# Kernel optimization log

Measured on AMD Instinct MI355X. Metric: run time of the kernel, lower is better.

## Reference

```python
import jax, jax.numpy as jnp
import numpy as np

N_E = 16384
SPLIT = (512, 512)
BETA = 0.25
K = 10
B = 4096


def _l2n(x):
    # F.normalize(p=2, dim=-1)
    return x * jax.lax.rsqrt(jnp.sum(x * x, axis=-1, keepdims=True) + 1e-12)


def _dist(x, y):
    return (jnp.sum(x * x, axis=1, keepdims=True)
            + jnp.sum(y * y, axis=1)
            - 2.0 * jnp.einsum('bd,nd->bn', x, y))


def _usage(idx):
    counts = jnp.zeros((N_E,), jnp.float32).at[idx.reshape(-1)].add(1.0)
    return jnp.sum(counts > 0).astype(jnp.float32) / N_E


def _soft_topk(d, emb):
    # smallest-K distances -> softmax(-values) weighted codebook mix
    neg_vals, idx = jax.lax.top_k(-d, K)            # [B, K]
    w = jax.nn.softmax(neg_vals, axis=1)            # softmax(-values)
    z_q = jnp.einsum('bk,bkd->bd', w, emb[idx])     # gather + weighted sum
    return z_q, idx


def _losses(z_q, z):
    vq = jnp.mean((z_q - jax.lax.stop_gradient(z)) ** 2)
    commit = BETA * jnp.mean((jax.lax.stop_gradient(z_q) - z) ** 2)
    return vq, commit


def setup_inputs() -> dict:
    key = jax.random.key(0)
    ks = jax.random.split(key, 5)
    u = 1.0 / N_E
    return {
        'z': jax.random.normal(ks[0], (B, sum(SPLIT)), jnp.float32),
        'w_text': jax.random.uniform(ks[1], (N_E, SPLIT[0]), jnp.float32, -u, u),
        'w_graph': jax.random.uniform(ks[2], (N_E, SPLIT[1]), jnp.float32, -u, u),
        'w_shared_text': jax.random.uniform(ks[3], (N_E, SPLIT[0]), jnp.float32, -u, u),
        'w_shared_graph': jax.random.uniform(ks[4], (N_E, SPLIT[1]), jnp.float32, -u, u),
    }


def reference(z, w_text, w_graph, w_shared_text, w_shared_graph):
    z_text, z_graph = jnp.split(z, [SPLIT[0]], axis=-1)

    # ---- shared codebook (joint text+graph distance) ----
    zt_n, zg_n = _l2n(z_text), _l2n(z_graph)
    wst_n, wsg_n = _l2n(w_shared_text), _l2n(w_shared_graph)
    d_shared = _dist(zt_n, wst_n) + 1.0 * _dist(zg_n, wsg_n)
    shared_emb = jnp.concatenate([wst_n, wsg_n], axis=-1)
    zq_s, idx_s = _soft_topk(d_shared, shared_emb)
    vq_s, com_s = _losses(zq_s, z)
    zq_s = z + jax.lax.stop_gradient(zq_s - z)      # straight-through
    usage_s = _usage(idx_s)

    # ---- text-specific codebook ----
    wt_n = _l2n(w_text)
    d_t = _dist(zt_n, wt_n)
    zq_t, idx_t = _soft_topk(d_t, wt_n)
    vq_t, com_t = _losses(zq_t, z_text)
    zq_t = z_text + jax.lax.stop_gradient(zq_t - z_text)
    usage_t = _usage(idx_t)

    # ---- graph-specific codebook ----
    wg_n = _l2n(w_graph)
    d_g = _dist(zg_n, wg_n)
    zq_g, idx_g = _soft_topk(d_g, wg_n)
    vq_g, com_g = _losses(zq_g, z_graph)
    zq_g = z_graph + jax.lax.stop_gradient(zq_g - z_graph)
    usage_g = _usage(idx_g)

    shared_text_emb, shared_graph_emb = jnp.split(zq_s, [SPLIT[0]], axis=-1)
    return (zq_s, shared_text_emb, shared_graph_emb, zq_t, zq_g,
            vq_s, com_s, vq_t, com_t, vq_g, com_g,
            usage_s, usage_t, usage_g)
```

## Files before the change

### kernel.cpp

```cpp
#include <hip/hip_runtime.h>
#include <stdint.h>

#define NE      16384
#define BATCH   4096
#define DFULL   1024
#define DHALF   512
#define TOPK    10
#define NCHUNK  16
#define CHUNK   1024
#define CPC     40
#define NCAND   (NCHUNK * CPC)
#define MRES    24
#define BETA_C  0.25f
#define CD1     ((size_t)BATCH * NCAND)

#define O1 ((size_t)BATCH * DFULL)
#define O2 (O1 + (size_t)BATCH * DHALF)
#define O3 (O2 + (size_t)BATCH * DHALF)
#define O4 (O3 + (size_t)BATCH * DHALF)
#define O5 (O4 + (size_t)BATCH * DHALF)

typedef __bf16 bf16x8 __attribute__((ext_vector_type(8)));
typedef float  f32x4  __attribute__((ext_vector_type(4)));

__device__ inline uint16_t f2bf(float f) {
    unsigned u = __float_as_uint(f);
    unsigned r = (u + 0x7FFFu + ((u >> 16) & 1u)) >> 16;
    return (uint16_t)r;
}
__device__ inline float bf2f(uint16_t u) {
    return __uint_as_float(((unsigned)u) << 16);
}
__device__ inline float dot8bf(uint4 e, const float* zp) {
    float s;
    s  = __uint_as_float(e.x << 16)          * zp[0];
    s += __uint_as_float(e.x & 0xFFFF0000u)  * zp[1];
    s += __uint_as_float(e.y << 16)          * zp[2];
    s += __uint_as_float(e.y & 0xFFFF0000u)  * zp[3];
    s += __uint_as_float(e.z << 16)          * zp[4];
    s += __uint_as_float(e.z & 0xFFFF0000u)  * zp[5];
    s += __uint_as_float(e.w << 16)          * zp[6];
    s += __uint_as_float(e.w & 0xFFFF0000u)  * zp[7];
    return s;
}

__global__ __launch_bounds__(256) void k_norm_z(const float* __restrict__ z,
                                                uint16_t* __restrict__ zn,
                                                float* __restrict__ rnzt,
                                                float* __restrict__ rnzg) {
    int b = blockIdx.x, t = threadIdx.x;
    const float4* zp = (const float4*)(z + (size_t)b * DFULL);
    float4 v = zp[t];
    float ss = v.x*v.x + v.y*v.y + v.z*v.z + v.w*v.w;
    #pragma unroll
    for (int off = 32; off; off >>= 1) ss += __shfl_xor(ss, off);
    __shared__ float red[4];
    if ((t & 63) == 0) red[t >> 6] = ss;
    __syncthreads();
    float tot = (t < 128) ? (red[0] + red[1]) : (red[2] + red[3]);
    float rn = rsqrtf(tot + 1e-12f);
    if (t == 0)   rnzt[b] = rn;
    if (t == 128) rnzg[b] = rn;
    uint16_t* o = zn + (size_t)b * DFULL + t * 4;
    o[0] = f2bf(v.x * rn); o[1] = f2bf(v.y * rn);
    o[2] = f2bf(v.z * rn); o[3] = f2bf(v.w * rn);
}

__global__ __launch_bounds__(128) void k_norm_cb_all(
    const float* __restrict__ w_st, const float* __restrict__ w_sg,
    const float* __restrict__ w_t,  const float* __restrict__ w_g,
    uint16_t* __restrict__ wsh, uint16_t* __restrict__ wt, uint16_t* __restrict__ wg,
    float* __restrict__ rns ) {
    int r = blockIdx.x, t = threadIdx.x, y = blockIdx.y;
    const float* w; uint16_t* dst; int dstld; float* rn_;
    if (y == 0)      { w = w_st; dst = wsh;       dstld = DFULL; rn_ = rns; }
    else if (y == 1) { w = w_sg; dst = wsh + 512; dstld = DFULL; rn_ = rns + NE; }
    else if (y == 2) { w = w_t;  dst = wt;        dstld = DHALF; rn_ = rns + 2 * NE; }
    else             { w = w_g;  dst = wg;        dstld = DHALF; rn_ = rns + 3 * NE; }
    const float4* wp = (const float4*)(w + (size_t)r * DHALF);
    float4 v = wp[t];
    float ss = v.x*v.x + v.y*v.y + v.z*v.z + v.w*v.w;
    #pragma unroll
    for (int off = 32; off; off >>= 1) ss += __shfl_xor(ss, off);
    __shared__ float red[2];
    if ((t & 63) == 0) red[t >> 6] = ss;
    __syncthreads();
    float rn = rsqrtf(red[0] + red[1] + 1e-12f);
    if (t == 0) rn_[r] = rn;
    uint16_t* o = dst + (size_t)r * dstld + t * 4;
    o[0] = f2bf(v.x * rn); o[1] = f2bf(v.y * rn);
    o[2] = f2bf(v.z * rn); o[3] = f2bf(v.w * rn);
}

__global__ __launch_bounds__(512, 4) void k_gemm_topk(
    const uint16_t* __restrict__ Zn,
    const uint16_t* __restrict__ wshn, const uint16_t* __restrict__ wtn,
    const uint16_t* __restrict__ wgn,
    unsigned* __restrict__ cand)
{
    __shared__ uint16_t Wsm[2][128 * 64];
    __shared__ uint16_t Zsm[2][128 * 64];

    const int tid  = threadIdx.x;
    const int lane = tid & 63;
    const int wv   = tid >> 6;
    const int wr   = wv >> 2;
    const int wc   = wv & 3;
    const int q    = lane >> 4;
    const int c    = lane & 15;
    const int rowbase  = blockIdx.y * 128;
    const int entchunk = blockIdx.x * CHUNK;
    const int gz = blockIdx.z;

    const uint16_t* Wn; int ldw, KT, zoff; unsigned* cdst;
    if (gz == 0)      { Wn = wshn; ldw = DFULL; KT = 16; zoff = 0;   cdst = cand; }
    else if (gz == 1) { Wn = wtn;  ldw = DHALF; KT = 8;  zoff = 0;   cdst = cand + CD1; }
    else              { Wn = wgn;  ldw = DHALF; KT = 8;  zoff = 512; cdst = cand + 2 * CD1; }
    const int ldz = DFULL;

    int sw_o0, sw_o1, sz_o0, sz_o1;
    int lw_o0, lw_o1, lz_o0, lz_o1;
    {
        int o, row, kb;
        o = (0 * 8 + wv) * 1024 + lane * 16; row = o >> 7; kb = (o & 127) ^ ((row & 7) << 4);
        sw_o0 = row * (ldw * 2) + kb; lw_o0 = o;
        sz_o0 = row * (ldz * 2) + kb; lz_o0 = o;
        o = (1 * 8 + wv) * 1024 + lane * 16; row = o >> 7; kb = (o & 127) ^ ((row & 7) << 4);
        sw_o1 = row * (ldw * 2) + kb; lw_o1 = o;
        sz_o1 = row * (ldz * 2) + kb; lz_o1 = o;
    }

    const char* Wbase = (const char*)Wn;
    const char* Zbase = (const char*)(Zn + zoff);

    unsigned La0 = 0, La1 = 0, La2 = 0, La3 = 0, La4 = 0;
    unsigned Lb0 = 0, Lb1 = 0, Lb2 = 0, Lb3 = 0, Lb4 = 0;

    uint4 sw0, sw1, sz0, sz1;

#define LOADG(cb2, kt2) {                                                           \
        const char* Wg = Wbase + ((size_t)(entchunk + (cb2) * 128) * ldw + (kt2) * 64) * 2; \
        const char* Zg = Zbase + ((size_t)rowbase * ldz + (kt2) * 64) * 2;          \
        sw0 = *(const uint4*)(Wg + sw_o0);                                          \
        sw1 = *(const uint4*)(Wg + sw_o1);                                          \
        sz0 = *(const uint4*)(Zg + sz_o0);                                          \
        sz1 = *(const uint4*)(Zg + sz_o1);                                          \
    }
#define WRITES(bufi) {                                                              \
        char* Wd = (char*)&Wsm[bufi][0];                                            \
        char* Zd = (char*)&Zsm[bufi][0];                                            \
        *(uint4*)(Wd + lw_o0) = sw0;                                                \
        *(uint4*)(Wd + lw_o1) = sw1;                                                \
        *(uint4*)(Zd + lz_o0) = sz0;                                                \
        *(uint4*)(Zd + lz_o1) = sz1;                                                \
    }

    LOADG(0, 0);
    WRITES(0);
    __syncthreads();
    int cur = 0;

    for (int cb = 0; cb < 8; ++cb) {
        f32x4 acc[4][2];
        #pragma unroll
        for (int m = 0; m < 4; ++m)
            #pragma unroll
            for (int n = 0; n < 2; ++n)
                acc[m][n] = (f32x4){0.f, 0.f, 0.f, 0.f};

        for (int kt = 0; kt < KT; ++kt) {
            int last = (kt + 1 == KT);
            int ncb = last ? cb + 1 : cb;
            int nkt = last ? 0 : kt + 1;
            int havenext = (ncb < 8);
            if (havenext) LOADG(ncb, nkt);

            const char* Wb = (const char*)&Wsm[cur][0];
            const char* Zb = (const char*)&Zsm[cur][0];
            #pragma unroll
            for (int ks = 0; ks < 2; ++ks) {
                int kb = ks * 64 + q * 16;
                bf16x8 b[2];
                #pragma unroll
                for (int n = 0; n < 2; ++n) {
                    int rb = wc * 32 + n * 16 + c;
                    b[n] = *(const bf16x8*)(Zb + rb * 128 + (kb ^ ((rb & 7) << 4)));
                }
                #pragma unroll
                for (int m = 0; m < 4; ++m) {
                    int ra = wr * 64 + m * 16 + c;
                    bf16x8 a = *(const bf16x8*)(Wb + ra * 128 + (kb ^ ((ra & 7) << 4)));
                    #pragma unroll
                    for (int n = 0; n < 2; ++n)
                        acc[m][n] = __builtin_amdgcn_mfma_f32_16x16x32_bf16(
                                        a, b[n], acc[m][n], 0, 0, 0);
                }
            }

            if (havenext) WRITES(cur ^ 1);
            __syncthreads();
            cur ^= 1;
        }

        const int entbase = entchunk + cb * 128 + wr * 64 + q * 4;
        #pragma unroll
        for (int n = 0; n < 2; ++n) {
            #pragma unroll
            for (int m = 0; m < 4; ++m) {
                #pragma unroll
                for (int i = 0; i < 4; ++i) {
                    unsigned u  = __float_as_uint(acc[m][n][i]);
                    unsigned mg = (unsigned)((int)u >> 31);
                    unsigned h  = (u >> 16) ^ (mg | 0x8000u);
                    unsigned p  = (h << 16) | (unsigned)(entbase + m * 16 + i);
                    if (n == 0) {
                        bool g0 = p > La0, g1 = p > La1, g2 = p > La2,
                             g3 = p > La3, g4 = p > La4;
                        La4 = g4 ? (g3 ? La3 : p) : La4;
                        La3 = g3 ? (g2 ? La2 : p) : La3;
                        La2 = g2 ? (g1 ? La1 : p) : La2;
                        La1 = g1 ? (g0 ? La0 : p) : La1;
                        La0 = g0 ? p : La0;
                    } else {
                        bool g0 = p > Lb0, g1 = p > Lb1, g2 = p > Lb2,
                             g3 = p > Lb3, g4 = p > Lb4;
                        Lb4 = g4 ? (g3 ? Lb3 : p) : Lb4;
                        Lb3 = g3 ? (g2 ? Lb2 : p) : Lb3;
                        Lb2 = g2 ? (g1 ? Lb1 : p) : Lb2;
                        Lb1 = g1 ? (g0 ? Lb0 : p) : Lb1;
                        Lb0 = g0 ? p : Lb0;
                    }
                }
            }
        }
    }

    {
        int grow = rowbase + wc * 32 + 0 * 16 + c;
        unsigned* dst = cdst + ((size_t)grow * NCHUNK + blockIdx.x) * CPC + wr * 20 + q * 5;
        dst[0] = La0; dst[1] = La1; dst[2] = La2; dst[3] = La3; dst[4] = La4;
        grow = rowbase + wc * 32 + 1 * 16 + c;
        dst = cdst + ((size_t)grow * NCHUNK + blockIdx.x) * CPC + wr * 20 + q * 5;
        dst[0] = Lb0; dst[1] = Lb1; dst[2] = Lb2; dst[3] = Lb3; dst[4] = Lb4;
    }
#undef LOADG
#undef WRITES
}

__global__ __launch_bounds__(256) void k_merge_all(
    const unsigned* __restrict__ cand,
    const uint16_t* __restrict__ wshn, const uint16_t* __restrict__ wtn,
    const uint16_t* __restrict__ wgn,
    const float* __restrict__ rnzt, const float* __restrict__ rnzg,
    const float* __restrict__ z, float* __restrict__ out,
    unsigned int* __restrict__ bm, float* __restrict__ ls)
{
    const int b = blockIdx.x, g = blockIdx.y, tid = threadIdx.x;
    const int lane = tid & 63, wv = tid >> 6;

    const unsigned* cd; const uint16_t* emb;
    int zoff, ld;
    float *outm, *outs1, *outs2;
    float rz0, rz1;
    if (g == 0) {
        cd = cand;           emb = wshn; zoff = 0;   ld = DFULL;
        outm = out; outs1 = out + O1; outs2 = out + O2;
        rz0 = rnzt[b]; rz1 = rnzg[b];
    } else if (g == 1) {
        cd = cand + CD1;     emb = wtn;  zoff = 0;   ld = DHALF;
        outm = out + O3; outs1 = nullptr; outs2 = nullptr;
        rz0 = rnzt[b]; rz1 = 0.f;
    } else {
        cd = cand + 2 * CD1; emb = wgn;  zoff = 512; ld = DHALF;
        outm = out + O4; outs1 = nullptr; outs2 = nullptr;
        rz0 = rnzg[b]; rz1 = 0.f;
    }
    unsigned int* bitmap = bm + g * (NE / 32);
    float* lossacc = ls + g;

    __shared__ float zsh[DFULL];
    __shared__ unsigned scand[MRES];
    __shared__ float ssh[MRES];
    __shared__ float wts[TOPK];
    __shared__ int   ish[TOPK];
    __shared__ float serr[4];

    const float* zrow = z + (size_t)b * DFULL + zoff;
    for (int cc = tid; cc < ld / 4; cc += 256)
        ((float4*)zsh)[cc] = ((const float4*)zrow)[cc];

    if (wv == 0) {
        unsigned creg[10];
        const unsigned* cb_ = cd + (size_t)b * NCAND;
        #pragma unroll
        for (int j = 0; j < 10; ++j) creg[j] = cb_[lane + 64 * j];
        for (int k = 0; k < MRES; ++k) {
            unsigned bv = 0;
            #pragma unroll
            for (int j = 0; j < 10; ++j) bv = (creg[j] > bv) ? creg[j] : bv;
            #pragma unroll
            for (int off = 32; off; off >>= 1) {
                unsigned ov = __shfl_xor(bv, off);
                bv = (ov > bv) ? ov : bv;
            }
            #pragma unroll
            for (int j = 0; j < 10; ++j) if (creg[j] == bv) creg[j] = 0u;
            if (lane == 0) scand[k] = bv;
        }
    }
    __syncthreads();

    for (int cc = wv; cc < MRES; cc += 4) {
        int idx = scand[cc] & 0xFFFFu;
        const uint16_t* er = emb + (size_t)idx * ld;
        uint4 e0 = *(const uint4*)(er + lane * 8);
        float t = rz0 * dot8bf(e0, zsh + lane * 8);
        if (ld == DFULL) {
            uint4 e1 = *(const uint4*)(er + 512 + lane * 8);
            t += rz1 * dot8bf(e1, zsh + 512 + lane * 8);
        }
        #pragma unroll
        for (int off = 32; off; off >>= 1) t += __shfl_xor(t, off);
        if (lane == 0) ssh[cc] = t;
    }
    __syncthreads();

    if (wv == 0) {
        float val = (lane < MRES) ? ssh[lane] : -1e30f;
        float vk[TOPK]; int sk[TOPK];
        #pragma unroll
        for (int k = 0; k < TOPK; ++k) {
            float v = val; int who = lane;
            #pragma unroll
            for (int off = 32; off; off >>= 1) {
                float ov = __shfl_xor(v, off);
                int   ow = __shfl_xor(who, off);
                if (ov > v || (ov == v && ow < who)) { v = ov; who = ow; }
            }
            vk[k] = v; sk[k] = who;
            if (lane == who) val = -1e30f;
        }
        if (lane == 0) {
            float vmax = vk[0], e[TOPK], sum = 0.f;
            #pragma unroll
            for (int k = 0; k < TOPK; ++k) { e[k] = expf(2.f * (vk[k] - vmax)); sum += e[k]; }
            #pragma unroll
            for (int k = 0; k < TOPK; ++k) {
                float w = e[k] / sum;
                int idx = scand[sk[k]] & 0xFFFFu;
                ish[k] = idx;
                wts[k] = w;
                atomicOr(&bitmap[idx >> 5], 1u << (idx & 31));
            }
        }
    }
    __syncthreads();

    float wk[TOPK]; int ik[TOPK];
    #pragma unroll
    for (int k = 0; k < TOPK; ++k) { wk[k] = wts[k]; ik[k] = ish[k]; }

    float err = 0.f;
    const int ng = ld / 4;
    for (int g2 = tid; g2 < ng; g2 += 256) {
        float ax = 0.f, ay = 0.f, az = 0.f, aw = 0.f;
        #pragma unroll
        for (int k = 0; k < TOPK; ++k) {
            ushort4 e = ((const ushort4*)(emb + (size_t)ik[k] * ld))[g2];
            float wv_ = wk[k];
            ax += wv_ * bf2f(e.x); ay += wv_ * bf2f(e.y);
            az += wv_ * bf2f(e.z); aw += wv_ * bf2f(e.w);
        }
        float4 zz = ((const float4*)zsh)[g2];
        float dx = ax - zz.x, dy = ay - zz.y, dz_ = az - zz.z, dw = aw - zz.w;
        err += dx*dx + dy*dy + dz_*dz_ + dw*dw;
        float4 a4 = {ax, ay, az, aw};
        ((float4*)(outm + (size_t)b * ld))[g2] = a4;
        if (outs1) {
            if (g2 < 128) ((float4*)(outs1 + (size_t)b * DHALF))[g2] = a4;
            else          ((float4*)(outs2 + (size_t)b * DHALF))[g2 - 128] = a4;
        }
    }
    #pragma unroll
    for (int off = 32; off; off >>= 1) err += __shfl_xor(err, off);
    if (lane == 0) serr[wv] = err;
    __syncthreads();
    if (tid == 0) atomicAdd(lossacc, serr[0] + serr[1] + serr[2] + serr[3]);
}

__global__ __launch_bounds__(256) void k_scalars(const unsigned int* __restrict__ bm,
                                                 const float* __restrict__ lossacc,
                                                 float* __restrict__ out)
{
    __shared__ float red[4];
    int tid = threadIdx.x;
    float counts[3];
    for (int g = 0; g < 3; ++g) {
        unsigned c = 0;
        for (int w = tid; w < NE / 32; w += 256) c += __popc(bm[g * (NE / 32) + w]);
        float f = (float)c;
        #pragma unroll
        for (int off = 32; off; off >>= 1) f += __shfl_xor(f, off);
        if ((tid & 63) == 0) red[tid >> 6] = f;
        __syncthreads();
        counts[g] = red[0] + red[1] + red[2] + red[3];
        __syncthreads();
    }
    if (tid == 0) {
        float vq_s = lossacc[0] / (4096.f * 1024.f);
        float vq_t = lossacc[1] / (4096.f * 512.f);
        float vq_g = lossacc[2] / (4096.f * 512.f);
        out[0] = vq_s; out[1] = BETA_C * vq_s;
        out[2] = vq_t; out[3] = BETA_C * vq_t;
        out[4] = vq_g; out[5] = BETA_C * vq_g;
        out[6] = counts[0] / (float)NE;
        out[7] = counts[1] / (float)NE;
        out[8] = counts[2] / (float)NE;
    }
}

extern "C" void kernel_launch(void* const* d_in, const int* in_sizes, int n_in,
                              void* d_out, int out_size, void* d_ws, size_t ws_size,
                              hipStream_t stream) {
    const float* z    = (const float*)d_in[0];
    const float* w_t  = (const float*)d_in[1];
    const float* w_g  = (const float*)d_in[2];
    const float* w_st = (const float*)d_in[3];
    const float* w_sg = (const float*)d_in[4];
    float* out = (float*)d_out;

    uint8_t* ws = (uint8_t*)d_ws;
    const size_t OFF_ZN  = 0;
    const size_t OFF_WSH = OFF_ZN  + (size_t)BATCH * DFULL * 2;
    const size_t OFF_WT  = OFF_WSH + (size_t)NE * DFULL * 2;
    const size_t OFF_WG  = OFF_WT  + (size_t)NE * DHALF * 2;
    const size_t OFF_CD  = OFF_WG  + (size_t)NE * DHALF * 2;
    const size_t OFF_RN  = OFF_CD  + (size_t)3 * BATCH * NCAND * 4;
    const size_t OFF_RNZ = OFF_RN  + (size_t)4 * NE * 4;
    const size_t OFF_BM  = OFF_RNZ + (size_t)2 * BATCH * 4;
    const size_t OFF_LS  = OFF_BM  + (size_t)3 * (NE / 8);

    uint16_t* zn   = (uint16_t*)(ws + OFF_ZN);
    uint16_t* wsh  = (uint16_t*)(ws + OFF_WSH);
    uint16_t* wt   = (uint16_t*)(ws + OFF_WT);
    uint16_t* wg   = (uint16_t*)(ws + OFF_WG);
    unsigned* cd   = (unsigned*)(ws + OFF_CD);
    float*    rns  = (float*)(ws + OFF_RN);
    float*    rnzt = (float*)(ws + OFF_RNZ);
    float*    rnzg = rnzt + BATCH;
    unsigned* bm   = (unsigned*)(ws + OFF_BM);
    float*    ls   = (float*)(ws + OFF_LS);

    hipMemsetAsync(ws + OFF_BM, 0, 3 * (NE / 8) + 64, stream);

    k_norm_z<<<BATCH, 256, 0, stream>>>(z, zn, rnzt, rnzg);
    k_norm_cb_all<<<dim3(NE, 4), 128, 0, stream>>>(w_st, w_sg, w_t, w_g,
                                                   wsh, wt, wg, rns);

    k_gemm_topk<<<dim3(NCHUNK, BATCH / 128, 3), 512, 0, stream>>>(zn, wsh, wt, wg, cd);

    k_merge_all<<<dim3(BATCH, 3), 256, 0, stream>>>(
        cd, wsh, wt, wg, rnzt, rnzg, z, out, bm, ls);

    k_scalars<<<1, 256, 0, stream>>>(bm, ls, out + O5);
}
```

Measured before the change: 620.4 us.

## Double batch-row tile of fused GEMM+topk kernel to 256 rows per block

Each block now covers 256 batch rows instead of 128, and each wave computes a 64x64 accumulator tile (4x4 MFMA fragments) instead of 64x32. The intent is to reuse every loaded codebook tile across twice as many rows, halving codebook traffic from global and LDS and raising MFMA work per A-fragment load. In exchange, register pressure roughly doubles (accumulators plus four top-5 lists), launch bounds drop to 2 blocks per CU, and the grid has half as many blocks, which lowers occupancy and the latency hiding it provides.

```diff
diff --git a/kernel.cpp b/kernel.cpp
--- a/kernel.cpp
+++ b/kernel.cpp
@@ -92,14 +92,14 @@
     o[2] = f2bf(v.z * rn); o[3] = f2bf(v.w * rn);
 }
 
-__global__ __launch_bounds__(512, 4) void k_gemm_topk(
+__global__ __launch_bounds__(512, 2) void k_gemm_topk(
     const uint16_t* __restrict__ Zn,
     const uint16_t* __restrict__ wshn, const uint16_t* __restrict__ wtn,
     const uint16_t* __restrict__ wgn,
     unsigned* __restrict__ cand)
 {
     __shared__ uint16_t Wsm[2][128 * 64];
-    __shared__ uint16_t Zsm[2][128 * 64];
+    __shared__ uint16_t Zsm[2][256 * 64];
 
     const int tid  = threadIdx.x;
     const int lane = tid & 63;
@@ -108,7 +108,7 @@
     const int wc   = wv & 3;
     const int q    = lane >> 4;
     const int c    = lane & 15;
-    const int rowbase  = blockIdx.y * 128;
+    const int rowbase  = blockIdx.y * 256;
     const int entchunk = blockIdx.x * CHUNK;
     const int gz = blockIdx.z;
 
@@ -118,8 +118,8 @@
     else              { Wn = wgn;  ldw = DHALF; KT = 8;  zoff = 512; cdst = cand + 2 * CD1; }
     const int ldz = DFULL;
 
-    int sw_o0, sw_o1, sz_o0, sz_o1;
-    int lw_o0, lw_o1, lz_o0, lz_o1;
+    int sw_o0, sw_o1, lw_o0, lw_o1;
+    int sz_o0, sz_o1, sz_o2, sz_o3, lz_o0, lz_o1, lz_o2, lz_o3;
     {
         int o, row, kb;
         o = (0 * 8 + wv) * 1024 + lane * 16; row = o >> 7; kb = (o & 127) ^ ((row & 7) << 4);
@@ -128,6 +128,10 @@
         o = (1 * 8 + wv) * 1024 + lane * 16; row = o >> 7; kb = (o & 127) ^ ((row & 7) << 4);
         sw_o1 = row * (ldw * 2) + kb; lw_o1 = o;
         sz_o1 = row * (ldz * 2) + kb; lz_o1 = o;
+        o = (2 * 8 + wv) * 1024 + lane * 16; row = o >> 7; kb = (o & 127) ^ ((row & 7) << 4);
+        sz_o2 = row * (ldz * 2) + kb; lz_o2 = o;
+        o = (3 * 8 + wv) * 1024 + lane * 16; row = o >> 7; kb = (o & 127) ^ ((row & 7) << 4);
+        sz_o3 = row * (ldz * 2) + kb; lz_o3 = o;
     }
 
     const char* Wbase = (const char*)Wn;
@@ -135,8 +139,10 @@
 
     unsigned La0 = 0, La1 = 0, La2 = 0, La3 = 0, La4 = 0;
     unsigned Lb0 = 0, Lb1 = 0, Lb2 = 0, Lb3 = 0, Lb4 = 0;
-
-    uint4 sw0, sw1, sz0, sz1;
+    unsigned Lc0 = 0, Lc1 = 0, Lc2 = 0, Lc3 = 0, Lc4 = 0;
+    unsigned Ld0 = 0, Ld1 = 0, Ld2 = 0, Ld3 = 0, Ld4 = 0;
+
+    uint4 sw0, sw1, sz0, sz1, sz2, sz3;
 
 #define LOADG(cb2, kt2) {                                                           \
         const char* Wg = Wbase + ((size_t)(entchunk + (cb2) * 128) * ldw + (kt2) * 64) * 2; \
@@ -145,6 +151,8 @@
         sw1 = *(const uint4*)(Wg + sw_o1);                                          \
         sz0 = *(const uint4*)(Zg + sz_o0);                                          \
         sz1 = *(const uint4*)(Zg + sz_o1);                                          \
+        sz2 = *(const uint4*)(Zg + sz_o2);                                          \
+        sz3 = *(const uint4*)(Zg + sz_o3);                                          \
     }
 #define WRITES(bufi) {                                                              \
         char* Wd = (char*)&Wsm[bufi][0];                                            \
@@ -153,6 +161,17 @@
         *(uint4*)(Wd + lw_o1) = sw1;                                                \
         *(uint4*)(Zd + lz_o0) = sz0;                                                \
         *(uint4*)(Zd + lz_o1) = sz1;                                                \
+        *(uint4*)(Zd + lz_o2) = sz2;                                                \
+        *(uint4*)(Zd + lz_o3) = sz3;                                                \
+    }
+#define INS5(p, X0, X1, X2, X3, X4) {                                               \
+        bool g0 = (p) > X0, g1 = (p) > X1, g2 = (p) > X2,                           \
+             g3 = (p) > X3, g4 = (p) > X4;                                          \
+        X4 = g4 ? (g3 ? X3 : (p)) : X4;                                             \
+        X3 = g3 ? (g2 ? X2 : (p)) : X3;                                             \
+        X2 = g2 ? (g1 ? X1 : (p)) : X2;                                             \
+        X1 = g1 ? (g0 ? X0 : (p)) : X1;                                             \
+        X0 = g0 ? (p) : X0;                                                         \
     }
 
     LOADG(0, 0);
@@ -161,11 +180,11 @@
     int cur = 0;
 
     for (int cb = 0; cb < 8; ++cb) {
-        f32x4 acc[4][2];
+        f32x4 acc[4][4];
         #pragma unroll
         for (int m = 0; m < 4; ++m)
             #pragma unroll
-            for (int n = 0; n < 2; ++n)
+            for (int n = 0; n < 4; ++n)
                 acc[m][n] = (f32x4){0.f, 0.f, 0.f, 0.f};
 
         for (int kt = 0; kt < KT; ++kt) {
@@ -180,10 +199,10 @@
             #pragma unroll
             for (int ks = 0; ks < 2; ++ks) {
                 int kb = ks * 64 + q * 16;
-                bf16x8 b[2];
+                bf16x8 b[4];
                 #pragma unroll
-                for (int n = 0; n < 2; ++n) {
-                    int rb = wc * 32 + n * 16 + c;
+                for (int n = 0; n < 4; ++n) {
+                    int rb = wc * 64 + n * 16 + c;
                     b[n] = *(const bf16x8*)(Zb + rb * 128 + (kb ^ ((rb & 7) << 4)));
                 }
                 #pragma unroll
@@ -191,7 +210,7 @@
                     int ra = wr * 64 + m * 16 + c;
                     bf16x8 a = *(const bf16x8*)(Wb + ra * 128 + (kb ^ ((ra & 7) << 4)));
                     #pragma unroll
-                    for (int n = 0; n < 2; ++n)
+                    for (int n = 0; n < 4; ++n)
                         acc[m][n] = __builtin_amdgcn_mfma_f32_16x16x32_bf16(
                                         a, b[n], acc[m][n], 0, 0, 0);
                 }
@@ -204,7 +223,7 @@
 
         const int entbase = entchunk + cb * 128 + wr * 64 + q * 4;
         #pragma unroll
-        for (int n = 0; n < 2; ++n) {
+        for (int n = 0; n < 4; ++n) {
             #pragma unroll
             for (int m = 0; m < 4; ++m) {
                 #pragma unroll
@@ -213,38 +232,34 @@
                     unsigned mg = (unsigned)((int)u >> 31);
                     unsigned h  = (u >> 16) ^ (mg | 0x8000u);
                     unsigned p  = (h << 16) | (unsigned)(entbase + m * 16 + i);
-                    if (n == 0) {
-                        bool g0 = p > La0, g1 = p > La1, g2 = p > La2,
-                             g3 = p > La3, g4 = p > La4;
-                        La4 = g4 ? (g3 ? La3 : p) : La4;
-                        La3 = g3 ? (g2 ? La2 : p) : La3;
-                        La2 = g2 ? (g1 ? La1 : p) : La2;
-                        La1 = g1 ? (g0 ? La0 : p) : La1;
-                        La0 = g0 ? p : La0;
-                    } else {
-                        bool g0 = p > Lb0, g1 = p > Lb1, g2 = p > Lb2,
-                             g3 = p > Lb3, g4 = p > Lb4;
-                        Lb4 = g4 ? (g3 ? Lb3 : p) : Lb4;
-                        Lb3 = g3 ? (g2 ? Lb2 : p) : Lb3;
-                        Lb2 = g2 ? (g1 ? Lb1 : p) : Lb2;
-                        Lb1 = g1 ? (g0 ? Lb0 : p) : Lb1;
-                        Lb0 = g0 ? p : Lb0;
-                    }
+                    if (n == 0)      { INS5(p, La0, La1, La2, La3, La4); }
+                    else if (n == 1) { INS5(p, Lb0, Lb1, Lb2, Lb3, Lb4); }
+                    else if (n == 2) { INS5(p, Lc0, Lc1, Lc2, Lc3, Lc4); }
+                    else             { INS5(p, Ld0, Ld1, Ld2, Ld3, Ld4); }
                 }
             }
         }
     }
 
     {
-        int grow = rowbase + wc * 32 + 0 * 16 + c;
-        unsigned* dst = cdst + ((size_t)grow * NCHUNK + blockIdx.x) * CPC + wr * 20 + q * 5;
+        unsigned* dst;
+        int grow;
+        grow = rowbase + wc * 64 + 0 * 16 + c;
+        dst = cdst + ((size_t)grow * NCHUNK + blockIdx.x) * CPC + wr * 20 + q * 5;
         dst[0] = La0; dst[1] = La1; dst[2] = La2; dst[3] = La3; dst[4] = La4;
-        grow = rowbase + wc * 32 + 1 * 16 + c;
+        grow = rowbase + wc * 64 + 1 * 16 + c;
         dst = cdst + ((size_t)grow * NCHUNK + blockIdx.x) * CPC + wr * 20 + q * 5;
         dst[0] = Lb0; dst[1] = Lb1; dst[2] = Lb2; dst[3] = Lb3; dst[4] = Lb4;
+        grow = rowbase + wc * 64 + 2 * 16 + c;
+        dst = cdst + ((size_t)grow * NCHUNK + blockIdx.x) * CPC + wr * 20 + q * 5;
+        dst[0] = Lc0; dst[1] = Lc1; dst[2] = Lc2; dst[3] = Lc3; dst[4] = Lc4;
+        grow = rowbase + wc * 64 + 3 * 16 + c;
+        dst = cdst + ((size_t)grow * NCHUNK + blockIdx.x) * CPC + wr * 20 + q * 5;
+        dst[0] = Ld0; dst[1] = Ld1; dst[2] = Ld2; dst[3] = Ld3; dst[4] = Ld4;
     }
 #undef LOADG
 #undef WRITES
+#undef INS5
 }
 
 __global__ __launch_bounds__(256) void k_merge_all(
@@ -457,7 +472,7 @@
     k_norm_cb_all<<<dim3(NE, 4), 128, 0, stream>>>(w_st, w_sg, w_t, w_g,
                                                    wsh, wt, wg, rns);
 
-    k_gemm_topk<<<dim3(NCHUNK, BATCH / 128, 3), 512, 0, stream>>>(zn, wsh, wt, wg, cd);
+    k_gemm_topk<<<dim3(NCHUNK, BATCH / 256, 3), 512, 0, stream>>>(zn, wsh, wt, wg, cd);
 
     k_merge_all<<<dim3(BATCH, 3), 256, 0, stream>>>(
         cd, wsh, wt, wg, rnzt, rnzg, z, out, bm, ls);
```

New measurement: 631.2 us. Within noise of the previous version (+1.7%).
